# Optimization experiments

Measured on AMD Instinct MI355X. Metric: run time of the kernel, lower is better.

The kernel has to match this reference:

```python
import jax, jax.numpy as jnp
import numpy as np

EPS_GAUSS = 1e-15
EPS_SOFTMAX = 1e-16

N, F, M, K = 200000, 256, 128, 8
ATT = 128
NUM_GRAPHS = 1024


def setup_inputs() -> dict:
    key = jax.random.key(0)
    ks = jax.random.split(key, 7)
    x = jax.random.normal(ks[0], (N, F), dtype=jnp.float32)
    # glorot-ish scales keep pre-gaussian activations in a sane range
    g = jax.random.normal(ks[1], (F, K * M), dtype=jnp.float32) * 0.05
    mu = jax.random.normal(ks[2], (K, M), dtype=jnp.float32) * 0.1
    sigma = jax.random.normal(ks[3], (K, M), dtype=jnp.float32) * 0.1
    w1 = jax.random.normal(ks[4], (ATT, M), dtype=jnp.float32) * 0.09
    w2 = jax.random.normal(ks[5], (1, ATT), dtype=jnp.float32) * 0.1
    batch = jnp.sort(jax.random.randint(ks[6], (N,), 0, NUM_GRAPHS, dtype=jnp.int64))
    return {"x": x, "g": g, "mu": mu, "sigma": sigma, "w1": w1,
            "w2": w2, "batch": batch, "num_graphs": NUM_GRAPHS}


def reference(x, g, mu, sigma, w1, w2, batch, num_graphs):
    n = x.shape[0]
    k, m = mu.shape
    # GMM "conv": dense matmul then Gaussian-mixture elementwise chain
    out = (x @ g).reshape(n, k, m)                       # [N, K, M]
    gauss = jnp.exp(-0.5 * (out - mu[None]) ** 2 / (EPS_GAUSS + sigma[None] ** 2))
    H = jnp.sum(out * gauss, axis=1)                     # [N, M]
    # attention pooling: scores per node
    a = jnp.tanh(H @ w1.T)                               # [N, ATT] (b1 unused in source)
    scores = a @ w2.T                                    # [N, 1]
    # segment (per-graph) softmax
    smax = jax.ops.segment_max(scores, batch, num_segments=num_graphs)
    e = jnp.exp(scores - smax[batch])
    ssum = jax.ops.segment_sum(e, batch, num_segments=num_graphs)
    S = e / (ssum[batch] + EPS_SOFTMAX)                  # [N, 1]
    # scatter_add pooling -> [num_graphs, M]
    return jax.ops.segment_sum(S * H, batch, num_segments=num_graphs)
```

## Files before the change

### kernel.cpp

```cpp
#include <hip/hip_runtime.h>
#include <hip/hip_bf16.h>
#include <hip/hip_fp16.h>
#include <math.h>

#define N_NODES 200000
#define FDIM    256
#define MDIM    128
#define KMIX    8
#define ATTD    128
#define NGRAPH  1024
#define TSN     64

typedef _Float16 half8 __attribute__((ext_vector_type(8)));
typedef _Float16 half4 __attribute__((ext_vector_type(4)));
typedef float    floatx4 __attribute__((ext_vector_type(4)));

__global__ __launch_bounds__(256) void pack_both(
    const float* __restrict__ g, const float* __restrict__ w1,
    _Float16* __restrict__ gh, _Float16* __restrict__ gl,
    _Float16* __restrict__ w1h, _Float16* __restrict__ w1l)
{
    if (blockIdx.x < 128) {
        int t    = blockIdx.x * 256 + threadIdx.x;
        int lane = t & 63;
        int frag = t >> 6;
        int fc   = frag & 7;
        int ctg  = (frag >> 3) & 7;
        int k    = frag >> 6;
        int col  = k * 128 + ctg * 16 + (lane & 15);
        int f0   = fc * 32 + (lane >> 4) * 8;
        half8 vh, vl;
        #pragma unroll
        for (int j = 0; j < 8; ++j) {
            float v = g[(size_t)(f0 + j) * 1024 + col];
            _Float16 h = (_Float16)v;
            vh[j] = h;
            vl[j] = (_Float16)(v - (float)h);
        }
        *(half8*)(gh + (size_t)t * 8) = vh;
        *(half8*)(gl + (size_t)t * 8) = vl;
    } else {
        int t    = (blockIdx.x - 128) * 256 + threadIdx.x;
        int lane = t & 63;
        int frag = t >> 6;
        int mc   = frag & 3;
        int ctg  = frag >> 2;
        int att  = ctg * 16 + (lane & 15);
        int m0   = mc * 32 + (lane >> 4) * 8;
        half8 vh, vl;
        #pragma unroll
        for (int j = 0; j < 8; ++j) {
            float v = w1[att * MDIM + m0 + j];
            _Float16 h = (_Float16)v;
            vh[j] = h;
            vl[j] = (_Float16)(v - (float)h);
        }
        *(half8*)(w1h + (size_t)t * 8) = vh;
        *(half8*)(w1l + (size_t)t * 8) = vl;
    }
}

__global__ __launch_bounds__(512, 4) void fused_forward(
    const float* __restrict__ x,
    const _Float16* __restrict__ gh, const _Float16* __restrict__ gl,
    const float* __restrict__ mu, const float* __restrict__ sigma,
    const _Float16* __restrict__ w1h, const _Float16* __restrict__ w1l,
    const float* __restrict__ w2,
    float* __restrict__ Hout, float* __restrict__ scores)
{
    __shared__ unsigned char smem[64 * 264 * 2 * 2 + 512];
    _Float16* xs_h = (_Float16*)smem;
    _Float16* xs_l = xs_h + 64 * 264;
    float*    Hs   = (float*)smem;
    float*    spart = (float*)(smem + 64 * 264 * 2 * 2);

    const int tid   = threadIdx.x;
    const int nBase = blockIdx.x * TSN;

    {
        const float4* xg = (const float4*)x;
        #pragma unroll
        for (int r = 0; r < 8; ++r) {
            int idx  = r * 512 + tid;
            int row  = idx >> 6;
            int quad = idx & 63;
            float4 v = xg[(size_t)(nBase + row) * 64 + quad];
            half4 h, l;
            h[0] = (_Float16)v.x; l[0] = (_Float16)(v.x - (float)h[0]);
            h[1] = (_Float16)v.y; l[1] = (_Float16)(v.y - (float)h[1]);
            h[2] = (_Float16)v.z; l[2] = (_Float16)(v.z - (float)h[2]);
            h[3] = (_Float16)v.w; l[3] = (_Float16)(v.w - (float)h[3]);
            *(half4*)&xs_h[row * 264 + quad * 4] = h;
            *(half4*)&xs_l[row * 264 + quad * 4] = l;
        }
    }
    __syncthreads();

    const int wave  = tid >> 6;
    const int lane  = tid & 63;
    const int c15   = lane & 15;
    const int q     = lane >> 4;
    const int nhalf = wave >> 2;
    const int colq  = wave & 3;

    float h[2][2][4];
    #pragma unroll
    for (int rt = 0; rt < 2; ++rt)
        #pragma unroll
        for (int ct = 0; ct < 2; ++ct)
            #pragma unroll
            for (int rg = 0; rg < 4; ++rg) h[rt][ct][rg] = 0.f;

    #pragma unroll 1
    for (int k = 0; k < KMIX; ++k) {
        __syncthreads();

        float muv[2], iv[2];
        #pragma unroll
        for (int ct = 0; ct < 2; ++ct) {
            int col = k * 128 + colq * 32 + ct * 16 + c15;
            muv[ct] = mu[col];
            float sg = sigma[col];
            iv[ct]  = 1.0f / (1e-15f + sg * sg);
        }

        floatx4 acc[2][2];
        #pragma unroll
        for (int rt = 0; rt < 2; ++rt)
            #pragma unroll
            for (int ct = 0; ct < 2; ++ct) acc[rt][ct] = (floatx4)0.f;

        #pragma unroll 2
        for (int fc = 0; fc < 8; ++fc) {
            const int f0 = fc * 32 + q * 8;
            half8 Ah[2], Al[2];
            #pragma unroll
            for (int rt = 0; rt < 2; ++rt) {
                int node = nhalf * 32 + rt * 16 + c15;
                Ah[rt] = *(const half8*)&xs_h[node * 264 + f0];
                Al[rt] = *(const half8*)&xs_l[node * 264 + f0];
            }
            half8 Bh[2], Bl[2];
            #pragma unroll
            for (int ct = 0; ct < 2; ++ct) {
                int ctg = colq * 2 + ct;
                size_t off = ((size_t)((k * 8 + ctg) * 8 + fc) * 64 + lane) * 8;
                Bh[ct] = *(const half8*)(gh + off);
                Bl[ct] = *(const half8*)(gl + off);
            }
            #pragma unroll
            for (int rt = 0; rt < 2; ++rt)
                #pragma unroll
                for (int ct = 0; ct < 2; ++ct) {
                    acc[rt][ct] = __builtin_amdgcn_mfma_f32_16x16x32_f16(Ah[rt], Bh[ct], acc[rt][ct], 0, 0, 0);
                    acc[rt][ct] = __builtin_amdgcn_mfma_f32_16x16x32_f16(Ah[rt], Bl[ct], acc[rt][ct], 0, 0, 0);
                    acc[rt][ct] = __builtin_amdgcn_mfma_f32_16x16x32_f16(Al[rt], Bh[ct], acc[rt][ct], 0, 0, 0);
                }
        }

        #pragma unroll
        for (int ct = 0; ct < 2; ++ct) {
            #pragma unroll
            for (int rt = 0; rt < 2; ++rt)
                #pragma unroll
                for (int rg = 0; rg < 4; ++rg) {
                    float o = acc[rt][ct][rg];
                    float d = o - muv[ct];
                    h[rt][ct][rg] += o * __expf(-0.5f * d * d * iv[ct]);
                }
        }
    }

    __syncthreads();
    const int HS_LD = MDIM + 4;
    #pragma unroll
    for (int rt = 0; rt < 2; ++rt)
        #pragma unroll
        for (int ct = 0; ct < 2; ++ct)
            #pragma unroll
            for (int rg = 0; rg < 4; ++rg) {
                int n = nhalf * 32 + rt * 16 + q * 4 + rg;
                int m = colq * 32 + ct * 16 + c15;
                Hs[n * HS_LD + m] = h[rt][ct][rg];
            }
    __syncthreads();

    #pragma unroll
    for (int r = 0; r < 4; ++r) {
        int idx  = r * 512 + tid;
        int node = idx >> 5;
        int mq   = idx & 31;
        float4 v = *(const float4*)&Hs[node * HS_LD + mq * 4];
        *(float4*)&Hout[(size_t)(nBase + node) * MDIM + mq * 4] = v;
    }

    {
        floatx4 datt[2][2];
        #pragma unroll
        for (int rt = 0; rt < 2; ++rt)
            #pragma unroll
            for (int ct = 0; ct < 2; ++ct) datt[rt][ct] = (floatx4)0.f;

        #pragma unroll
        for (int mc = 0; mc < 4; ++mc) {
            half8 Ahh[2], All[2];
            #pragma unroll
            for (int rt = 0; rt < 2; ++rt) {
                int node = nhalf * 32 + rt * 16 + c15;
                const float* hp = &Hs[node * HS_LD + mc * 32 + q * 8];
                #pragma unroll
                for (int j = 0; j < 8; ++j) {
                    float v = hp[j];
                    _Float16 hi = (_Float16)v;
                    Ahh[rt][j] = hi;
                    All[rt][j] = (_Float16)(v - (float)hi);
                }
            }
            #pragma unroll
            for (int ct = 0; ct < 2; ++ct) {
                int frag = (colq * 2 + ct) * 4 + mc;
                size_t off = ((size_t)frag * 64 + lane) * 8;
                half8 Bhh = *(const half8*)(w1h + off);
                half8 Bll = *(const half8*)(w1l + off);
                #pragma unroll
                for (int rt = 0; rt < 2; ++rt) {
                    datt[rt][ct] = __builtin_amdgcn_mfma_f32_16x16x32_f16(Ahh[rt], Bhh, datt[rt][ct], 0, 0, 0);
                    datt[rt][ct] = __builtin_amdgcn_mfma_f32_16x16x32_f16(Ahh[rt], Bll, datt[rt][ct], 0, 0, 0);
                    datt[rt][ct] = __builtin_amdgcn_mfma_f32_16x16x32_f16(All[rt], Bhh, datt[rt][ct], 0, 0, 0);
                }
            }
        }

        float w2v[2];
        #pragma unroll
        for (int ct = 0; ct < 2; ++ct) w2v[ct] = w2[colq * 32 + ct * 16 + c15];

        #pragma unroll
        for (int rt = 0; rt < 2; ++rt) {
            #pragma unroll
            for (int rg = 0; rg < 4; ++rg) {
                float p = 0.f;
                #pragma unroll
                for (int ct = 0; ct < 2; ++ct) {
                    float dot = datt[rt][ct][rg];
                    float e2 = __expf(2.f * dot);
                    float av = 1.f - 2.f / (e2 + 1.f);
                    p = fmaf(av, w2v[ct], p);
                }
                p += __shfl_xor(p, 1);
                p += __shfl_xor(p, 2);
                p += __shfl_xor(p, 4);
                p += __shfl_xor(p, 8);
                if (c15 == 0) {
                    int n = nhalf * 32 + rt * 16 + q * 4 + rg;
                    spart[n * 4 + colq] = p;
                }
            }
        }
    }
    __syncthreads();
    if (tid < 64) {
        const float* sp = &spart[tid * 4];
        scores[nBase + tid] = (sp[0] + sp[1]) + (sp[2] + sp[3]);
    }
}

#define CHUNK 1024
__global__ __launch_bounds__(256) void segment_pool(
    const float* __restrict__ H, const float* __restrict__ scores,
    const int* __restrict__ batch, float* __restrict__ out)
{
    const int gidx = blockIdx.x >> 1;
    const int mh   = blockIdx.x & 1;
    const int tid  = threadIdx.x;

    int lo = 0, hi = N_NODES;
    while (lo < hi) { int mid = (lo + hi) >> 1; if (batch[mid] <  gidx) lo = mid + 1; else hi = mid; }
    const int start = lo;
    hi = N_NODES;
    while (lo < hi) { int mid = (lo + hi) >> 1; if (batch[mid] <= gidx) lo = mid + 1; else hi = mid; }
    const int end = lo;

    __shared__ float red[4];
    __shared__ float ebuf[CHUNK];
    __shared__ float part[16][64];

    float mx = -INFINITY;
    for (int i = start + tid; i < end; i += 256) mx = fmaxf(mx, scores[i]);
    #pragma unroll
    for (int o = 32; o > 0; o >>= 1) mx = fmaxf(mx, __shfl_xor(mx, o));
    if ((tid & 63) == 0) red[tid >> 6] = mx;
    __syncthreads();
    mx = fmaxf(fmaxf(red[0], red[1]), fmaxf(red[2], red[3]));
    __syncthreads();

    const int mq = tid & 15;
    const int p  = tid >> 4;
    const float* Hb = H + mh * 64;
    float4 acc = make_float4(0.f, 0.f, 0.f, 0.f);
    float ls = 0.f;

    for (int c0 = start; c0 < end; c0 += CHUNK) {
        const int clen = min(end - c0, CHUNK);
        __syncthreads();
        for (int i = tid; i < clen; i += 256) {
            float e = __expf(scores[c0 + i] - mx);
            ebuf[i] = e;
            ls += e;
        }
        __syncthreads();
        for (int i = p; i < clen; i += 16) {
            float e = ebuf[i];
            const float4 hv = *(const float4*)&Hb[(size_t)(c0 + i) * MDIM + mq * 4];
            acc.x = fmaf(e, hv.x, acc.x);
            acc.y = fmaf(e, hv.y, acc.y);
            acc.z = fmaf(e, hv.z, acc.z);
            acc.w = fmaf(e, hv.w, acc.w);
        }
    }

    #pragma unroll
    for (int o = 32; o > 0; o >>= 1) ls += __shfl_xor(ls, o);
    if ((tid & 63) == 0) red[tid >> 6] = ls;
    part[p][mq * 4 + 0] = acc.x;
    part[p][mq * 4 + 1] = acc.y;
    part[p][mq * 4 + 2] = acc.z;
    part[p][mq * 4 + 3] = acc.w;
    __syncthreads();
    if (tid < 64) {
        float s = red[0] + red[1] + red[2] + red[3];
        const float inv = 1.f / (s + 1e-16f);
        float a = 0.f;
        #pragma unroll
        for (int pp = 0; pp < 16; ++pp) a += part[pp][tid];
        out[gidx * MDIM + mh * 64 + tid] = a * inv;
    }
}

extern "C" void kernel_launch(void* const* d_in, const int* in_sizes, int n_in,
                              void* d_out, int out_size, void* d_ws, size_t ws_size,
                              hipStream_t stream)
{
    const float* x     = (const float*)d_in[0];
    const float* g     = (const float*)d_in[1];
    const float* mu    = (const float*)d_in[2];
    const float* sigma = (const float*)d_in[3];
    const float* w1    = (const float*)d_in[4];
    const float* w2    = (const float*)d_in[5];
    const int*   batch = (const int*)d_in[6];
    float* out = (float*)d_out;

    float*    H      = (float*)d_ws;
    float*    scores = H + (size_t)N_NODES * MDIM;
    _Float16* ghp    = (_Float16*)(scores + N_NODES);
    _Float16* glp    = ghp + (size_t)FDIM * KMIX * MDIM;
    _Float16* w1hp   = glp + (size_t)FDIM * KMIX * MDIM;
    _Float16* w1lp   = w1hp + (size_t)ATTD * MDIM;

    pack_both<<<136, 256, 0, stream>>>(g, w1, ghp, glp, w1hp, w1lp);
    fused_forward<<<N_NODES / TSN, 512, 0, stream>>>(x, ghp, glp, mu, sigma,
                                                     w1hp, w1lp, w2, H, scores);
    segment_pool<<<NGRAPH * 2, 256, 0, stream>>>(H, scores, batch, out);
}
```

Measured before the change: 662.7 us.

## Fuse segment softmax pooling into forward kernel via atomics, drop H round-trip

The fused forward kernel now computes exp(score) per node and accumulates per-graph sums of e and e·H directly with atomicAdd, using the sorted batch ids in shared memory. A tiny normalize kernel then divides the two sums. This removes the full N×M H write and re-read and the binary-search segment_pool kernel. In exchange it drops the segment-max subtraction, which relies on scores being bounded (tanh outputs times w2), and adds atomic contention and non-deterministic summation order.

```diff
diff --git a/kernel.cpp b/kernel.cpp
--- a/kernel.cpp
+++ b/kernel.cpp
@@ -15,10 +15,11 @@
 typedef _Float16 half4 __attribute__((ext_vector_type(4)));
 typedef float    floatx4 __attribute__((ext_vector_type(4)));
 
-__global__ __launch_bounds__(256) void pack_both(
+__global__ __launch_bounds__(256) void pack_zero(
     const float* __restrict__ g, const float* __restrict__ w1,
     _Float16* __restrict__ gh, _Float16* __restrict__ gl,
-    _Float16* __restrict__ w1h, _Float16* __restrict__ w1l)
+    _Float16* __restrict__ w1h, _Float16* __restrict__ w1l,
+    float* __restrict__ acc)
 {
     if (blockIdx.x < 128) {
         int t    = blockIdx.x * 256 + threadIdx.x;
@@ -39,7 +40,7 @@
         }
         *(half8*)(gh + (size_t)t * 8) = vh;
         *(half8*)(gl + (size_t)t * 8) = vl;
-    } else {
+    } else if (blockIdx.x < 136) {
         int t    = (blockIdx.x - 128) * 256 + threadIdx.x;
         int lane = t & 63;
         int frag = t >> 6;
@@ -57,6 +58,9 @@
         }
         *(half8*)(w1h + (size_t)t * 8) = vh;
         *(half8*)(w1l + (size_t)t * 8) = vl;
+    } else {
+        int i = (blockIdx.x - 136) * 256 + threadIdx.x;
+        if (i < NGRAPH * (MDIM + 1)) acc[i] = 0.f;
     }
 }
 
@@ -65,14 +69,17 @@
     const _Float16* __restrict__ gh, const _Float16* __restrict__ gl,
     const float* __restrict__ mu, const float* __restrict__ sigma,
     const _Float16* __restrict__ w1h, const _Float16* __restrict__ w1l,
-    const float* __restrict__ w2,
-    float* __restrict__ Hout, float* __restrict__ scores)
+    const float* __restrict__ w2, const int* __restrict__ batch,
+    float* __restrict__ sumE, float* __restrict__ sumEH)
 {
-    __shared__ unsigned char smem[64 * 264 * 2 * 2 + 512];
+    __shared__ unsigned char smem[64 * 264 * 2 * 2];
     _Float16* xs_h = (_Float16*)smem;
     _Float16* xs_l = xs_h + 64 * 264;
     float*    Hs   = (float*)smem;
-    float*    spart = (float*)(smem + 64 * 264 * 2 * 2);
+    float*    tail = (float*)(smem + 64 * 264 * 2);
+    float*    spart = tail;
+    float*    esc   = tail + 256;
+    int*      bseg  = (int*)(tail + 320);
 
     const int tid   = threadIdx.x;
     const int nBase = blockIdx.x * TSN;
@@ -183,16 +190,8 @@
                 int m = colq * 32 + ct * 16 + c15;
                 Hs[n * HS_LD + m] = h[rt][ct][rg];
             }
-    __syncthreads();
-
-    #pragma unroll
-    for (int r = 0; r < 4; ++r) {
-        int idx  = r * 512 + tid;
-        int node = idx >> 5;
-        int mq   = idx & 31;
-        float4 v = *(const float4*)&Hs[node * HS_LD + mq * 4];
-        *(float4*)&Hout[(size_t)(nBase + node) * MDIM + mq * 4] = v;
-    }
+    if (tid < 64) bseg[tid] = batch[nBase + tid];
+    __syncthreads();
 
     {
         floatx4 datt[2][2];
@@ -261,80 +260,49 @@
     __syncthreads();
     if (tid < 64) {
         const float* sp = &spart[tid * 4];
-        scores[nBase + tid] = (sp[0] + sp[1]) + (sp[2] + sp[3]);
+        float s = (sp[0] + sp[1]) + (sp[2] + sp[3]);
+        esc[tid] = __expf(s);
+    }
+    __syncthreads();
+
+    {
+        const int col = tid & 127;
+        const int grp = tid >> 7;
+        const int n0  = grp * 16;
+        float partial = 0.f;
+        int cur = bseg[n0];
+        #pragma unroll 1
+        for (int i = 0; i < 16; ++i) {
+            int n = n0 + i;
+            int b = bseg[n];
+            if (b != cur) {
+                atomicAdd(&sumEH[(size_t)cur * MDIM + col], partial);
+                partial = 0.f; cur = b;
+            }
+            partial = fmaf(esc[n], Hs[n * HS_LD + col], partial);
+        }
+        atomicAdd(&sumEH[(size_t)cur * MDIM + col], partial);
+
+        if (tid < 64) {
+            bool lead = (tid == 0) || (bseg[tid] != bseg[tid - 1]);
+            if (lead) {
+                int b = bseg[tid];
+                float s = 0.f;
+                for (int j = tid; j < 64 && bseg[j] == b; ++j) s += esc[j];
+                atomicAdd(&sumE[b], s);
+            }
+        }
     }
 }
 
-#define CHUNK 1024
-__global__ __launch_bounds__(256) void segment_pool(
-    const float* __restrict__ H, const float* __restrict__ scores,
-    const int* __restrict__ batch, float* __restrict__ out)
+__global__ __launch_bounds__(256) void normalize_out(
+    const float* __restrict__ acc, float* __restrict__ out)
 {
-    const int gidx = blockIdx.x >> 1;
-    const int mh   = blockIdx.x & 1;
-    const int tid  = threadIdx.x;
-
-    int lo = 0, hi = N_NODES;
-    while (lo < hi) { int mid = (lo + hi) >> 1; if (batch[mid] <  gidx) lo = mid + 1; else hi = mid; }
-    const int start = lo;
-    hi = N_NODES;
-    while (lo < hi) { int mid = (lo + hi) >> 1; if (batch[mid] <= gidx) lo = mid + 1; else hi = mid; }
-    const int end = lo;
-
-    __shared__ float red[4];
-    __shared__ float ebuf[CHUNK];
-    __shared__ float part[16][64];
-
-    float mx = -INFINITY;
-    for (int i = start + tid; i < end; i += 256) mx = fmaxf(mx, scores[i]);
-    #pragma unroll
-    for (int o = 32; o > 0; o >>= 1) mx = fmaxf(mx, __shfl_xor(mx, o));
-    if ((tid & 63) == 0) red[tid >> 6] = mx;
-    __syncthreads();
-    mx = fmaxf(fmaxf(red[0], red[1]), fmaxf(red[2], red[3]));
-    __syncthreads();
-
-    const int mq = tid & 15;
-    const int p  = tid >> 4;
-    const float* Hb = H + mh * 64;
-    float4 acc = make_float4(0.f, 0.f, 0.f, 0.f);
-    float ls = 0.f;
-
-    for (int c0 = start; c0 < end; c0 += CHUNK) {
-        const int clen = min(end - c0, CHUNK);
-        __syncthreads();
-        for (int i = tid; i < clen; i += 256) {
-            float e = __expf(scores[c0 + i] - mx);
-            ebuf[i] = e;
-            ls += e;
-        }
-        __syncthreads();
-        for (int i = p; i < clen; i += 16) {
-            float e = ebuf[i];
-            const float4 hv = *(const float4*)&Hb[(size_t)(c0 + i) * MDIM + mq * 4];
-            acc.x = fmaf(e, hv.x, acc.x);
-            acc.y = fmaf(e, hv.y, acc.y);
-            acc.z = fmaf(e, hv.z, acc.z);
-            acc.w = fmaf(e, hv.w, acc.w);
-        }
-    }
-
-    #pragma unroll
-    for (int o = 32; o > 0; o >>= 1) ls += __shfl_xor(ls, o);
-    if ((tid & 63) == 0) red[tid >> 6] = ls;
-    part[p][mq * 4 + 0] = acc.x;
-    part[p][mq * 4 + 1] = acc.y;
-    part[p][mq * 4 + 2] = acc.z;
-    part[p][mq * 4 + 3] = acc.w;
-    __syncthreads();
-    if (tid < 64) {
-        float s = red[0] + red[1] + red[2] + red[3];
-        const float inv = 1.f / (s + 1e-16f);
-        float a = 0.f;
-        #pragma unroll
-        for (int pp = 0; pp < 16; ++pp) a += part[pp][tid];
-        out[gidx * MDIM + mh * 64 + tid] = a * inv;
-    }
+    int i = blockIdx.x * 256 + threadIdx.x;
+    const float* sumE  = acc;
+    const float* sumEH = acc + NGRAPH;
+    float e = sumE[i >> 7];
+    out[i] = sumEH[i] / (e + 1e-30f);
 }
 
 extern "C" void kernel_launch(void* const* d_in, const int* in_sizes, int n_in,
@@ -350,15 +318,15 @@
     const int*   batch = (const int*)d_in[6];
     float* out = (float*)d_out;
 
-    float*    H      = (float*)d_ws;
-    float*    scores = H + (size_t)N_NODES * MDIM;
-    _Float16* ghp    = (_Float16*)(scores + N_NODES);
-    _Float16* glp    = ghp + (size_t)FDIM * KMIX * MDIM;
-    _Float16* w1hp   = glp + (size_t)FDIM * KMIX * MDIM;
-    _Float16* w1lp   = w1hp + (size_t)ATTD * MDIM;
-
-    pack_both<<<136, 256, 0, stream>>>(g, w1, ghp, glp, w1hp, w1lp);
+    float*    accp = (float*)d_ws;
+    _Float16* ghp  = (_Float16*)(accp + NGRAPH * (MDIM + 1));
+    _Float16* glp  = ghp + (size_t)FDIM * KMIX * MDIM;
+    _Float16* w1hp = glp + (size_t)FDIM * KMIX * MDIM;
+    _Float16* w1lp = w1hp + (size_t)ATTD * MDIM;
+
+    pack_zero<<<652, 256, 0, stream>>>(g, w1, ghp, glp, w1hp, w1lp, accp);
     fused_forward<<<N_NODES / TSN, 512, 0, stream>>>(x, ghp, glp, mu, sigma,
-                                                     w1hp, w1lp, w2, H, scores);
-    segment_pool<<<NGRAPH * 2, 256, 0, stream>>>(H, scores, batch, out);
+                                                     w1hp, w1lp, w2, batch,
+                                                     accp, accp + NGRAPH);
+    normalize_out<<<NGRAPH * MDIM / 256, 256, 0, stream>>>(accp, out);
 }
```

New measurement: 643.2 us. -2.9%, faster.
